# Performance work log

Measured on AMD Instinct MI355X. Metric: run time of the kernel, lower is better.

The kernel has to match this reference:

```python
import jax, jax.numpy as jnp
import numpy as np

S = 2048        # tokens (single prefill sequence)
HID = 3584      # hidden_size
H = 16          # num query heads
KV = 8          # num kv heads
D = 256         # head_dim
WINDOW = 1024   # sliding window size
CAP = 50.0      # logit softcap
SCALE = 256.0 ** -0.5   # query_pre_attn_scalar ** -0.5
THETA = 10000.0


def setup_inputs() -> dict:
    key = jax.random.key(0)
    ks = jax.random.split(key, 5)
    hidden_states = jax.random.normal(ks[0], (S, HID), dtype=jnp.float32)
    positions = jnp.arange(S, dtype=jnp.int32)
    Wq = jax.random.normal(ks[1], (HID, H * D), dtype=jnp.float32) * 0.02
    Wk = jax.random.normal(ks[2], (HID, KV * D), dtype=jnp.float32) * 0.02
    Wv = jax.random.normal(ks[3], (HID, KV * D), dtype=jnp.float32) * 0.02
    Wo = jax.random.normal(ks[4], (H * D, HID), dtype=jnp.float32) * 0.02
    return {"hidden_states": hidden_states, "positions": positions,
            "Wq": Wq, "Wk": Wk, "Wv": Wv, "Wo": Wo}


def _rope_neox(x, positions):
    # x: [S, n_heads, D]; neox-style: rotate halves, full rotary_dim == D
    half = D // 2
    inv_freq = 1.0 / (THETA ** (jnp.arange(0, half, dtype=jnp.float32) * 2.0 / D))
    freqs = positions.astype(jnp.float32)[:, None] * inv_freq[None, :]  # [S, half]
    cos = jnp.cos(freqs)[:, None, :].astype(x.dtype)
    sin = jnp.sin(freqs)[:, None, :].astype(x.dtype)
    x1, x2 = x[..., :half], x[..., half:]
    return jnp.concatenate([x1 * cos - x2 * sin, x2 * cos + x1 * sin], axis=-1)


def reference(hidden_states, positions, Wq, Wk, Wv, Wo):
    # QKV projections (no bias)
    q = (hidden_states @ Wq).reshape(S, H, D)
    k = (hidden_states @ Wk).reshape(S, KV, D)
    v = (hidden_states @ Wv).reshape(S, KV, D)
    q = _rope_neox(q, positions)
    k = _rope_neox(k, positions)
    # grouped-query attention: G query heads per kv head
    G = H // KV
    qg = q.reshape(S, KV, G, D)
    scores = jnp.einsum('qkgd,skd->kgqs', qg, k) * jnp.asarray(SCALE, q.dtype)
    # logit soft-capping
    scores = CAP * jnp.tanh(scores / CAP)
    # causal + sliding-window mask
    i = positions[:, None]
    j = positions[None, :]
    mask = (j <= i) & ((i - j) < WINDOW)   # [S, S]
    neg = jnp.finfo(scores.dtype).min
    scores = jnp.where(mask[None, None, :, :], scores, neg)
    p = jax.nn.softmax(scores, axis=-1)
    attn = jnp.einsum('kgqs,skd->qkgd', p, v).reshape(S, H * D)
    return attn @ Wo
```

## Files before the change

kernel.cpp:

```cpp
#include <hip/hip_runtime.h>
#include <stdint.h>

#define S 2048
#define HID 3584
#define NH 16
#define NKV 8
#define DH 256
#define WINDOW 1024
#define SCALE 0.0625f
#define CAP 50.0f

typedef short s16x8 __attribute__((ext_vector_type(8)));
typedef float f32x4 __attribute__((ext_vector_type(4)));

__device__ __forceinline__ short f2bf(float f) {
  union { float f; uint32_t u; } c; c.f = f;
  uint32_t u = c.u;
  uint32_t r = (u + 0x7FFFu + ((u >> 16) & 1u)) >> 16;
  return (short)r;
}
__device__ __forceinline__ float bf2f(short s) {
  union { uint32_t u; float f; } c;
  c.u = ((uint32_t)(uint16_t)s) << 16;
  return c.f;
}
__device__ __forceinline__ void gll16(const void* g, void* l) {
  __builtin_amdgcn_global_load_lds((const __attribute__((address_space(1))) void*)g,
                                   (__attribute__((address_space(3))) void*)l, 16, 0, 0);
}
#define BAR() asm volatile("s_barrier" ::: "memory")
#define VW6() asm volatile("s_waitcnt vmcnt(6)" ::: "memory")

__global__ void rope_table_kernel(float2* __restrict__ tbl) {
  int idx = blockIdx.x * 256 + threadIdx.x;
  int s = idx >> 7, i = idx & 127;
  float inv = __expf(-(float)i * (9.210340371976184f / 128.0f));
  float fr = (float)s * inv;
  tbl[idx] = make_float2(cosf(fr), sinf(fr));
}

__global__ void conv_hs_kernel(const float* __restrict__ src, short* __restrict__ dst) {
  int gid = blockIdx.x * 256 + threadIdx.x;
  float4 a = *(const float4*)&src[(size_t)gid * 8];
  float4 b = *(const float4*)&src[(size_t)gid * 8 + 4];
  s16x8 o;
  o[0] = f2bf(a.x); o[1] = f2bf(a.y); o[2] = f2bf(a.z); o[3] = f2bf(a.w);
  o[4] = f2bf(b.x); o[5] = f2bf(b.y); o[6] = f2bf(b.z); o[7] = f2bf(b.w);
  *(s16x8*)&dst[(size_t)gid * 8] = o;
}

__global__ __launch_bounds__(256)
void transpose_kernel(const float* __restrict__ src, short* __restrict__ dst,
                      int K, int N)
{
  __shared__ __align__(16) short t[64][76];
  int ntn = N >> 6;
  int tn = blockIdx.x % ntn, tk = blockIdx.x / ntn;
  int tid = threadIdx.x;
  int c = tid & 63, rg = tid >> 6;
  #pragma unroll
  for (int i = 0; i < 4; ++i) {
    int r0 = i * 16 + rg * 4;
    short tmp[4];
    #pragma unroll
    for (int j = 0; j < 4; ++j)
      tmp[j] = f2bf(src[(size_t)(tk * 64 + r0 + j) * N + tn * 64 + c]);
    *(short4*)&t[c][r0] = *(short4*)tmp;
  }
  __syncthreads();
  #pragma unroll
  for (int it = 0; it < 2; ++it) {
    int flat = it * 256 + tid;
    int n = flat >> 3, kc = flat & 7;
    *(s16x8*)&dst[(size_t)(tn * 64 + n) * K + tk * 64 + kc * 8] = *(s16x8*)&t[n][kc * 8];
  }
}

template<int BN, int KS>
__device__ __forceinline__ void gemm_ph(const short* __restrict__ srcA,
                                        const short* __restrict__ srcB,
                                        int tid, int NT,
                                        f32x4 (&acc)[8][BN / 64])
{
  constexpr int NFP = BN / 128;
  constexpr int BTILE = BN * 64;
  __shared__ __align__(16) short Asb[2 * 16384];
  __shared__ __align__(16) short Bsb[2 * BTILE];
  const int wv = tid >> 6, lane = tid & 63;
  const int lr = lane & 15, lk = lane >> 4;
  const int wm_id = wv >> 2, wn_id = wv & 3;
  const int r7 = lr & 7;
  const int abase = (wm_id * 128 + lr) * 64 + ((lk ^ r7) * 8);
  const int bbase = (wn_id * (BN / 4) + lr) * 64 + ((lk ^ r7) * 8);

  s16x8 af[4][2];
  s16x8 bfr[2][NFP][2];

  auto stA = [&](int ts, int r, int b) {
    gll16(srcA + (size_t)ts * 64 + (size_t)(r * 64) * KS,
          Asb + b * 16384 + r * 4096 + wv * 512);
  };
  auto stB = [&](int ts, int q, int b) {
    gll16(srcB + (size_t)ts * 64 + (size_t)(q * 64) * KS,
          Bsb + b * BTILE + q * 4096 + wv * 512);
  };
  auto LDA = [&](int mh, int b) {
    const short* A = Asb + b * 16384;
    #pragma unroll
    for (int mf = 0; mf < 4; ++mf)
      #pragma unroll
      for (int kh = 0; kh < 2; ++kh)
        af[mf][kh] = *(const s16x8*)&A[(abase + (mh * 64 + mf * 16) * 64) ^ (kh * 32)];
  };
  auto LDB = [&](int nh, int b) {
    const short* B = Bsb + b * BTILE;
    #pragma unroll
    for (int nf = 0; nf < NFP; ++nf)
      #pragma unroll
      for (int kh = 0; kh < 2; ++kh)
        bfr[nh][nf][kh] = *(const s16x8*)&B[(bbase + (nh * NFP + nf) * 16 * 64) ^ (kh * 32)];
  };
  auto MMA = [&](int mh, int nh) {
    asm volatile("s_waitcnt lgkmcnt(0)" ::: "memory");
    __builtin_amdgcn_sched_barrier(0);
    __builtin_amdgcn_s_setprio(1);
    #pragma unroll
    for (int mf = 0; mf < 4; ++mf)
      #pragma unroll
      for (int nf = 0; nf < NFP; ++nf) {
        acc[mh * 4 + mf][nh * NFP + nf] =
          __builtin_amdgcn_mfma_f32_16x16x32_bf16(af[mf][0], bfr[nh][nf][0],
                                                  acc[mh * 4 + mf][nh * NFP + nf], 0, 0, 0);
        acc[mh * 4 + mf][nh * NFP + nf] =
          __builtin_amdgcn_mfma_f32_16x16x32_bf16(af[mf][1], bfr[nh][nf][1],
                                                  acc[mh * 4 + mf][nh * NFP + nf], 0, 0, 0);
      }
    __builtin_amdgcn_s_setprio(0);
  };

  #pragma unroll
  for (int r = 0; r < 4; ++r) stA(0, r, 0);
  #pragma unroll
  for (int q = 0; q < BN / 64; ++q) stB(0, q, 0);
  #pragma unroll
  for (int r = 0; r < 4; ++r) stA(1, r, 1);
  stB(1, 0, 1); stB(1, 1, 1);
  asm volatile("s_waitcnt vmcnt(0)" ::: "memory");
  BAR();

  const int NI = NT / 2;
  for (int i = 0; i < NI; ++i) {
    const int T = 2 * i;
    const int t2 = (T + 2 < NT) ? T + 2 : NT - 2;
    const int t3 = (T + 3 < NT) ? T + 3 : NT - 1;
    LDA(0, 0); LDB(0, 0);
    if constexpr (BN == 256) { stB(T + 1, 2, 1); stB(T + 1, 3, 1); }
    BAR(); MMA(0, 0); BAR();
    LDB(1, 0);
    stA(t2, 0, 0); stA(t2, 2, 0);
    BAR(); MMA(0, 1); BAR();
    LDA(1, 0);
    stB(t2, 0, 0); stB(t2, 1, 0);
    BAR(); MMA(1, 0); BAR();
    stA(t2, 1, 0); stA(t2, 3, 0);
    VW6();
    BAR(); MMA(1, 1); BAR();
    LDA(0, 1); LDB(0, 1);
    if constexpr (BN == 256) { stB(t2, 2, 0); stB(t2, 3, 0); }
    BAR(); MMA(0, 0); BAR();
    LDB(1, 1);
    stA(t3, 0, 1); stA(t3, 2, 1);
    BAR(); MMA(0, 1); BAR();
    LDA(1, 1);
    stB(t3, 0, 1); stB(t3, 1, 1);
    BAR(); MMA(1, 0); BAR();
    stA(t3, 1, 1); stA(t3, 3, 1);
    VW6();
    BAR(); MMA(1, 1); BAR();
  }
  asm volatile("s_waitcnt vmcnt(0)" ::: "memory");
}

__global__ __launch_bounds__(512, 2)
void qkv_gemm8_kernel(const short* __restrict__ hsb, const short* __restrict__ Wt,
                      short* __restrict__ qb, short* __restrict__ kbuf,
                      short* __restrict__ vtb)
{
  int bid = blockIdx.x;
  int swz = (bid & 7) * 32 + (bid >> 3);
  int bm = swz >> 5, bn = swz & 31;
  int m0 = bm * 256, n0 = bn * 256;
  int tid = threadIdx.x;
  int row8 = tid >> 3;
  int colsw = ((tid & 7) ^ (row8 & 7)) * 8;
  const short* srcA = hsb + (size_t)(m0 + row8) * HID + colsw;
  const short* srcB = Wt + (size_t)(n0 + row8) * HID + colsw;
  f32x4 acc[8][4] = {};
  gemm_ph<256, HID>(srcA, srcB, tid, HID / 64, acc);

  int wv = tid >> 6, lane = tid & 63;
  int lr = lane & 15, lk = lane >> 4;
  int wm = (wv >> 2) * 128, wn = (wv & 3) * 64;
  int region = (n0 < 4096) ? 0 : ((n0 < 6144) ? 1 : 2);
  #pragma unroll
  for (int m = 0; m < 8; ++m) {
    int srow_b = m0 + wm + m * 16 + lk * 4;
    #pragma unroll
    for (int n = 0; n < 4; ++n) {
      int ncol = n0 + wn + n * 16 + lr;
      #pragma unroll
      for (int r = 0; r < 4; ++r) {
        int srow = srow_b + r;
        short bv = f2bf(acc[m][n][r]);
        if (region == 0) {
          int h = ncol >> 8, d = ncol & 255;
          qb[((size_t)h * S + srow) * DH + d] = bv;
        } else if (region == 1) {
          int c = ncol - 4096; int kv = c >> 8, d = c & 255;
          kbuf[((size_t)kv * S + srow) * DH + d] = bv;
        } else {
          int c = ncol - 6144; int kv = c >> 8, d = c & 255;
          vtb[((size_t)kv * DH + d) * S + srow] = bv;
        }
      }
    }
  }
}

__global__ __launch_bounds__(512, 2)
void out_gemm8_kernel(const short* __restrict__ attnb, const short* __restrict__ WtO,
                      float* __restrict__ out)
{
  int bid = blockIdx.x;
  int swz = (bid & 7) * 28 + (bid >> 3);
  int bm = swz / 28, bn = swz % 28;
  int m0 = bm * 256, n0 = bn * 128;
  int tid = threadIdx.x;
  int row8 = tid >> 3;
  int colsw = ((tid & 7) ^ (row8 & 7)) * 8;
  const short* srcA = attnb + (size_t)(m0 + row8) * 4096 + colsw;
  const short* srcB = WtO + (size_t)(n0 + row8) * 4096 + colsw;
  f32x4 acc[8][2] = {};
  gemm_ph<128, 4096>(srcA, srcB, tid, 4096 / 64, acc);

  int wv = tid >> 6, lane = tid & 63;
  int lr = lane & 15, lk = lane >> 4;
  int wm = (wv >> 2) * 128, wn = (wv & 3) * 32;
  #pragma unroll
  for (int m = 0; m < 8; ++m) {
    int srow_b = m0 + wm + m * 16 + lk * 4;
    #pragma unroll
    for (int n = 0; n < 2; ++n) {
      int ncol = n0 + wn + n * 16 + lr;
      #pragma unroll
      for (int r = 0; r < 4; ++r)
        out[(size_t)(srow_b + r) * HID + ncol] = acc[m][n][r];
    }
  }
}

__global__ void rope_kernel(short* __restrict__ qb, short* __restrict__ kbuf,
                            const float2* __restrict__ tbl)
{
  int gid = blockIdx.x * 256 + threadIdx.x;
  int row = gid >> 4, ch = gid & 15;
  short* base = (row < NH * S) ? (qb + (size_t)row * DH)
                               : (kbuf + (size_t)(row - NH * S) * DH);
  int s = row & (S - 1);
  int i0 = ch * 8;
  s16x8 x1 = *(s16x8*)(base + i0);
  s16x8 x2 = *(s16x8*)(base + 128 + i0);
  s16x8 y1, y2;
  #pragma unroll
  for (int j = 0; j < 8; ++j) {
    float2 cs = tbl[s * 128 + i0 + j];
    float a = bf2f(x1[j]), b = bf2f(x2[j]);
    y1[j] = f2bf(a * cs.x - b * cs.y);
    y2[j] = f2bf(b * cs.x + a * cs.y);
  }
  *(s16x8*)(base + i0) = y1;
  *(s16x8*)(base + 128 + i0) = y2;
}

__global__ __launch_bounds__(256)
void attn_kernel(const short* __restrict__ qb, const short* __restrict__ kbuf,
                 const short* __restrict__ vtb, short* __restrict__ attnb)
{
  __shared__ __align__(16) short Klds[64][256];
  __shared__ __align__(16) short Vlds[256][72];
  __shared__ __align__(16) short Plds[4][16][76];
  int bid = blockIdx.x;
  int qt = bid >> 4, h = bid & 15;
  int kv = h >> 1;
  int q0 = qt * 64;
  int tid = threadIdx.x, w = tid >> 6, lane = tid & 63;
  int lr = lane & 15, lk = lane >> 4;
  int qrow_base = q0 + w * 16;
  s16x8 qf[8];
  const short* qrow = qb + ((size_t)h * S + (qrow_base + lr)) * DH;
  #pragma unroll
  for (int kb = 0; kb < 8; ++kb)
    qf[kb] = *(const s16x8*)(qrow + kb * 32 + lk * 8);
  f32x4 acc_o[16] = {};
  float l_r[4] = {0.0f, 0.0f, 0.0f, 0.0f};
  int tlo = (q0 >= WINDOW - 1) ? ((q0 - (WINDOW - 1)) >> 6) : 0;
  int thi = q0 >> 6;
  const short* kbase = kbuf + (size_t)kv * S * DH;
  const short* vbase = vtb + (size_t)kv * DH * S;

  s16x8 kpf[8], vpf[8];
  auto loadRegs = [&](int t) {
    int k0 = t * 64;
    #pragma unroll
    for (int it = 0; it < 8; ++it) {
      int flat = it * 256 + tid;
      int r = flat >> 5, cg = flat & 31;
      kpf[it] = *(const s16x8*)(kbase + (size_t)(k0 + r) * DH + cg * 8);
    }
    #pragma unroll
    for (int it = 0; it < 8; ++it) {
      int flat = it * 256 + tid;
      int r = flat >> 3, cg = flat & 7;
      vpf[it] = *(const s16x8*)(vbase + (size_t)r * S + k0 + cg * 8);
    }
  };
  auto writeLds = [&]() {
    #pragma unroll
    for (int it = 0; it < 8; ++it) {
      int flat = it * 256 + tid;
      int r = flat >> 5, cg = flat & 31;
      *(s16x8*)&Klds[r][(cg ^ (r & 7)) * 8] = kpf[it];
    }
    #pragma unroll
    for (int it = 0; it < 8; ++it) {
      int flat = it * 256 + tid;
      int r = flat >> 3, cg = flat & 7;
      *(s16x8*)&Vlds[r][cg * 8] = vpf[it];
    }
  };

  loadRegs(tlo);
  for (int t = tlo; t <= thi; ++t) {
    int k0 = t * 64;
    writeLds();
    __syncthreads();
    if (t < thi) loadRegs(t + 1);
    f32x4 sc4[4] = {};
    __builtin_amdgcn_s_setprio(1);
    #pragma unroll
    for (int kb = 0; kb < 8; ++kb)
      #pragma unroll
      for (int ni = 0; ni < 4; ++ni) {
        int row = ni * 16 + lr;
        s16x8 b = *(const s16x8*)&Klds[row][(((kb << 2) | lk) ^ (row & 7)) * 8];
        sc4[ni] = __builtin_amdgcn_mfma_f32_16x16x32_bf16(qf[kb], b, sc4[ni], 0, 0, 0);
      }
    __builtin_amdgcn_s_setprio(0);
    bool interior = (k0 + 63 <= qrow_base) && (qrow_base + 15 - k0 < WINDOW);
    #pragma unroll
    for (int ni = 0; ni < 4; ++ni)
      #pragma unroll
      for (int r = 0; r < 4; ++r) {
        float raw = sc4[ni][r];
        float u = fabsf(raw) * (2.0f * SCALE / CAP);
        float e = __expf(-u);
        float th = (1.0f - e) / (1.0f + e);
        float z = CAP * copysignf(th, raw) - CAP;
        if (!interior) {
          int qg = qrow_base + lk * 4 + r;
          int kg = k0 + ni * 16 + lr;
          bool valid = (kg <= qg) && (qg - kg < WINDOW);
          z = valid ? z : -1e30f;
        }
        float p = __expf(z);
        sc4[ni][r] = p;
        l_r[r] += p;
      }
    #pragma unroll
    for (int ni = 0; ni < 4; ++ni)
      #pragma unroll
      for (int r = 0; r < 4; ++r)
        Plds[w][lk * 4 + r][ni * 16 + lr] = f2bf(sc4[ni][r]);
    s16x8 pa0 = *(const s16x8*)&Plds[w][lr][lk * 8];
    s16x8 pa1 = *(const s16x8*)&Plds[w][lr][32 + lk * 8];
    __builtin_amdgcn_s_setprio(1);
    #pragma unroll
    for (int df = 0; df < 16; ++df) {
      s16x8 b0 = *(const s16x8*)&Vlds[df * 16 + lr][lk * 8];
      s16x8 b1 = *(const s16x8*)&Vlds[df * 16 + lr][32 + lk * 8];
      acc_o[df] = __builtin_amdgcn_mfma_f32_16x16x32_bf16(pa0, b0, acc_o[df], 0, 0, 0);
      acc_o[df] = __builtin_amdgcn_mfma_f32_16x16x32_bf16(pa1, b1, acc_o[df], 0, 0, 0);
    }
    __builtin_amdgcn_s_setprio(0);
    __syncthreads();
  }
  #pragma unroll
  for (int r = 0; r < 4; ++r) {
    float lsum = l_r[r];
    #pragma unroll
    for (int off = 1; off < 16; off <<= 1)
      lsum += __shfl_xor(lsum, off, 64);
    float inv = 1.0f / lsum;
    int srow = qrow_base + lk * 4 + r;
    #pragma unroll
    for (int df = 0; df < 16; ++df)
      attnb[(size_t)srow * (NH * DH) + h * DH + df * 16 + lr] = f2bf(acc_o[df][r] * inv);
  }
}

extern "C" void kernel_launch(void* const* d_in, const int* in_sizes, int n_in,
                              void* d_out, int out_size, void* d_ws, size_t ws_size,
                              hipStream_t stream) {
  const float* hs = (const float*)d_in[0];
  const float* Wq = (const float*)d_in[2];
  const float* Wk = (const float*)d_in[3];
  const float* Wv = (const float*)d_in[4];
  const float* Wo = (const float*)d_in[5];
  float* out = (float*)d_out;
  char* ws = (char*)d_ws;
  size_t off = 0;
  float2* tbl  = (float2*)(ws + off); off += 2097152;
  short* qb    = (short*)(ws + off);  off += 16777216;
  short* kbuf  = (short*)(ws + off);  off += 8388608;
  short* vtb   = (short*)(ws + off);  off += 8388608;
  short* attnb = (short*)(ws + off);  off += 16777216;
  short* hsb   = (short*)(ws + off);  off += 14680064;
  short* Wt    = (short*)(ws + off);  off += 58720256;
  short* WtO   = (short*)(ws + off);  off += 29360128;

  hipLaunchKernelGGL(rope_table_kernel, dim3(1024), dim3(256), 0, stream, tbl);
  hipLaunchKernelGGL(conv_hs_kernel, dim3(3584), dim3(256), 0, stream, hs, hsb);
  hipLaunchKernelGGL(transpose_kernel, dim3(64 * 56), dim3(256), 0, stream,
                     Wq, Wt, HID, 4096);
  hipLaunchKernelGGL(transpose_kernel, dim3(32 * 56), dim3(256), 0, stream,
                     Wk, Wt + (size_t)4096 * HID, HID, 2048);
  hipLaunchKernelGGL(transpose_kernel, dim3(32 * 56), dim3(256), 0, stream,
                     Wv, Wt + (size_t)6144 * HID, HID, 2048);
  hipLaunchKernelGGL(transpose_kernel, dim3(56 * 64), dim3(256), 0, stream,
                     Wo, WtO, 4096, HID);
  hipLaunchKernelGGL(qkv_gemm8_kernel, dim3(256), dim3(512), 0, stream,
                     hsb, Wt, qb, kbuf, vtb);
  hipLaunchKernelGGL(rope_kernel, dim3(3072), dim3(256), 0, stream, qb, kbuf, tbl);
  hipLaunchKernelGGL(attn_kernel, dim3(512), dim3(256), 0, stream,
                     qb, kbuf, vtb, attnb);
  hipLaunchKernelGGL(out_gemm8_kernel, dim3(224), dim3(512), 0, stream,
                     attnb, WtO, out);
}
```

Baseline: 408.6 us.

## Double-buffer LDS fragment registers to overlap LDS reads with MFMA

The GEMM main loop now keeps two sets of A and B fragment registers. It issues the LDS reads for the next MMA sub-block before running the current MFMA batch, and drops the explicit lgkmcnt(0) wait at the start of each MMA. The aim is to hide LDS read latency behind matrix-core work instead of stalling before each batch. In exchange, more live fragment registers raise VGPR pressure under the 512x2 launch bound, which could cause spills or lower occupancy. Correctness now relies on compiler-inserted waits and on the buffer-reuse ordering across barriers.

```diff
diff --git a/kernel.cpp b/kernel.cpp
--- a/kernel.cpp
+++ b/kernel.cpp
@@ -93,8 +93,8 @@
   const int abase = (wm_id * 128 + lr) * 64 + ((lk ^ r7) * 8);
   const int bbase = (wn_id * (BN / 4) + lr) * 64 + ((lk ^ r7) * 8);
 
-  s16x8 af[4][2];
-  s16x8 bfr[2][NFP][2];
+  s16x8 afA[4][2], afB[4][2];
+  s16x8 bf0[NFP][2], bf1[NFP][2];
 
   auto stA = [&](int ts, int r, int b) {
     gll16(srcA + (size_t)ts * 64 + (size_t)(r * 64) * KS,
@@ -104,24 +104,23 @@
     gll16(srcB + (size_t)ts * 64 + (size_t)(q * 64) * KS,
           Bsb + b * BTILE + q * 4096 + wv * 512);
   };
-  auto LDA = [&](int mh, int b) {
+  auto RDA = [&](s16x8 (&dst)[4][2], int mh, int b) {
     const short* A = Asb + b * 16384;
     #pragma unroll
     for (int mf = 0; mf < 4; ++mf)
       #pragma unroll
       for (int kh = 0; kh < 2; ++kh)
-        af[mf][kh] = *(const s16x8*)&A[(abase + (mh * 64 + mf * 16) * 64) ^ (kh * 32)];
-  };
-  auto LDB = [&](int nh, int b) {
+        dst[mf][kh] = *(const s16x8*)&A[(abase + (mh * 64 + mf * 16) * 64) ^ (kh * 32)];
+  };
+  auto RDB = [&](s16x8 (&dst)[NFP][2], int nh, int b) {
     const short* B = Bsb + b * BTILE;
     #pragma unroll
     for (int nf = 0; nf < NFP; ++nf)
       #pragma unroll
       for (int kh = 0; kh < 2; ++kh)
-        bfr[nh][nf][kh] = *(const s16x8*)&B[(bbase + (nh * NFP + nf) * 16 * 64) ^ (kh * 32)];
-  };
-  auto MMA = [&](int mh, int nh) {
-    asm volatile("s_waitcnt lgkmcnt(0)" ::: "memory");
+        dst[nf][kh] = *(const s16x8*)&B[(bbase + (nh * NFP + nf) * 16 * 64) ^ (kh * 32)];
+  };
+  auto MMA = [&](s16x8 (&fa)[4][2], s16x8 (&fb)[NFP][2], int mh, int nh) {
     __builtin_amdgcn_sched_barrier(0);
     __builtin_amdgcn_s_setprio(1);
     #pragma unroll
@@ -129,10 +128,10 @@
       #pragma unroll
       for (int nf = 0; nf < NFP; ++nf) {
         acc[mh * 4 + mf][nh * NFP + nf] =
-          __builtin_amdgcn_mfma_f32_16x16x32_bf16(af[mf][0], bfr[nh][nf][0],
+          __builtin_amdgcn_mfma_f32_16x16x32_bf16(fa[mf][0], fb[nf][0],
                                                   acc[mh * 4 + mf][nh * NFP + nf], 0, 0, 0);
         acc[mh * 4 + mf][nh * NFP + nf] =
-          __builtin_amdgcn_mfma_f32_16x16x32_bf16(af[mf][1], bfr[nh][nf][1],
+          __builtin_amdgcn_mfma_f32_16x16x32_bf16(fa[mf][1], fb[nf][1],
                                                   acc[mh * 4 + mf][nh * NFP + nf], 0, 0, 0);
       }
     __builtin_amdgcn_s_setprio(0);
@@ -147,36 +146,53 @@
   stB(1, 0, 1); stB(1, 1, 1);
   asm volatile("s_waitcnt vmcnt(0)" ::: "memory");
   BAR();
+  RDA(afA, 0, 0); RDB(bf0, 0, 0);
 
   const int NI = NT / 2;
   for (int i = 0; i < NI; ++i) {
     const int T = 2 * i;
     const int t2 = (T + 2 < NT) ? T + 2 : NT - 2;
     const int t3 = (T + 3 < NT) ? T + 3 : NT - 1;
-    LDA(0, 0); LDB(0, 0);
     if constexpr (BN == 256) { stB(T + 1, 2, 1); stB(T + 1, 3, 1); }
-    BAR(); MMA(0, 0); BAR();
-    LDB(1, 0);
+    BAR();
+    RDB(bf1, 1, 0);
+    MMA(afA, bf0, 0, 0);
+    BAR();
     stA(t2, 0, 0); stA(t2, 2, 0);
-    BAR(); MMA(0, 1); BAR();
-    LDA(1, 0);
+    BAR();
+    RDA(afB, 1, 0);
+    MMA(afA, bf1, 0, 1);
+    BAR();
     stB(t2, 0, 0); stB(t2, 1, 0);
-    BAR(); MMA(1, 0); BAR();
+    BAR();
+    MMA(afB, bf0, 1, 0);
+    BAR();
     stA(t2, 1, 0); stA(t2, 3, 0);
     VW6();
-    BAR(); MMA(1, 1); BAR();
-    LDA(0, 1); LDB(0, 1);
+    BAR();
+    RDA(afA, 0, 1); RDB(bf0, 0, 1);
+    MMA(afB, bf1, 1, 1);
+    BAR();
     if constexpr (BN == 256) { stB(t2, 2, 0); stB(t2, 3, 0); }
-    BAR(); MMA(0, 0); BAR();
-    LDB(1, 1);
+    BAR();
+    RDB(bf1, 1, 1);
+    MMA(afA, bf0, 0, 0);
+    BAR();
     stA(t3, 0, 1); stA(t3, 2, 1);
-    BAR(); MMA(0, 1); BAR();
-    LDA(1, 1);
+    BAR();
+    RDA(afB, 1, 1);
+    MMA(afA, bf1, 0, 1);
+    BAR();
     stB(t3, 0, 1); stB(t3, 1, 1);
-    BAR(); MMA(1, 0); BAR();
+    BAR();
+    MMA(afB, bf0, 1, 0);
+    BAR();
     stA(t3, 1, 1); stA(t3, 3, 1);
     VW6();
-    BAR(); MMA(1, 1); BAR();
+    BAR();
+    RDA(afA, 0, 0); RDB(bf0, 0, 0);
+    MMA(afB, bf1, 1, 1);
+    BAR();
   }
   asm volatile("s_waitcnt vmcnt(0)" ::: "memory");
 }
```

After: 418.4 us. 2.4% more time.

## Split attention key tiles across two wave groups per block and merge results

Applied to the files above, without the earlier changes.

Each attention block now runs 512 threads split into two groups of four waves. The groups process alternating key tiles of the same query tile in separate LDS buffers, then combine their partial outputs and row sums through LDS at the end. This halves the serial key-tile loop per block to cut per-block latency. It also reverses the query-tile order so the heaviest tiles launch first, and swizzles the V LDS layout. The costs are double the LDS footprint, an extra combine pass, and possible register pressure or occupancy limits under the 512-thread launch bound.

```diff
diff --git a/kernel.cpp b/kernel.cpp
--- a/kernel.cpp
+++ b/kernel.cpp
@@ -282,20 +282,23 @@
   *(s16x8*)(base + 128 + i0) = y2;
 }
 
-__global__ __launch_bounds__(256)
+__global__ __launch_bounds__(512)
 void attn_kernel(const short* __restrict__ qb, const short* __restrict__ kbuf,
                  const short* __restrict__ vtb, short* __restrict__ attnb)
 {
-  __shared__ __align__(16) short Klds[64][256];
-  __shared__ __align__(16) short Vlds[256][72];
-  __shared__ __align__(16) short Plds[4][16][76];
+  __shared__ __align__(16) short Klds[2][64][256];
+  __shared__ __align__(16) short Vlds[2][256][72];
+  __shared__ __align__(16) short Plds[8][16][72];
   int bid = blockIdx.x;
-  int qt = bid >> 4, h = bid & 15;
+  int qt = 31 - (bid >> 4), h = bid & 15;
   int kv = h >> 1;
   int q0 = qt * 64;
-  int tid = threadIdx.x, w = tid >> 6, lane = tid & 63;
+  int tid = threadIdx.x;
+  int w = tid >> 6, lane = tid & 63;
+  int g = w >> 2, wsub = w & 3;
+  int gtid = tid & 255;
   int lr = lane & 15, lk = lane >> 4;
-  int qrow_base = q0 + w * 16;
+  int qrow_base = q0 + wsub * 16;
   s16x8 qf[8];
   const short* qrow = qb + ((size_t)h * S + (qrow_base + lr)) * DH;
   #pragma unroll
@@ -313,13 +316,13 @@
     int k0 = t * 64;
     #pragma unroll
     for (int it = 0; it < 8; ++it) {
-      int flat = it * 256 + tid;
+      int flat = it * 256 + gtid;
       int r = flat >> 5, cg = flat & 31;
       kpf[it] = *(const s16x8*)(kbase + (size_t)(k0 + r) * DH + cg * 8);
     }
     #pragma unroll
     for (int it = 0; it < 8; ++it) {
-      int flat = it * 256 + tid;
+      int flat = it * 256 + gtid;
       int r = flat >> 3, cg = flat & 7;
       vpf[it] = *(const s16x8*)(vbase + (size_t)r * S + k0 + cg * 8);
     }
@@ -327,84 +330,117 @@
   auto writeLds = [&]() {
     #pragma unroll
     for (int it = 0; it < 8; ++it) {
-      int flat = it * 256 + tid;
+      int flat = it * 256 + gtid;
       int r = flat >> 5, cg = flat & 31;
-      *(s16x8*)&Klds[r][(cg ^ (r & 7)) * 8] = kpf[it];
+      *(s16x8*)&Klds[g][r][(cg ^ (r & 7)) * 8] = kpf[it];
     }
     #pragma unroll
     for (int it = 0; it < 8; ++it) {
-      int flat = it * 256 + tid;
+      int flat = it * 256 + gtid;
       int r = flat >> 3, cg = flat & 7;
-      *(s16x8*)&Vlds[r][cg * 8] = vpf[it];
-    }
-  };
-
-  loadRegs(tlo);
-  for (int t = tlo; t <= thi; ++t) {
-    int k0 = t * 64;
-    writeLds();
+      *(s16x8*)&Vlds[g][r][(cg ^ (r & 7)) * 8] = vpf[it];
+    }
+  };
+
+  int tg0 = tlo + g;
+  int n_all = thi - tlo + 1;
+  int jmax = (n_all + 1) >> 1;
+  if (tg0 <= thi) loadRegs(tg0);
+  for (int j = 0; j < jmax; ++j) {
+    int t = tg0 + 2 * j;
+    bool active = (t <= thi);
+    if (active) writeLds();
     __syncthreads();
-    if (t < thi) loadRegs(t + 1);
-    f32x4 sc4[4] = {};
-    __builtin_amdgcn_s_setprio(1);
-    #pragma unroll
-    for (int kb = 0; kb < 8; ++kb)
-      #pragma unroll
-      for (int ni = 0; ni < 4; ++ni) {
-        int row = ni * 16 + lr;
-        s16x8 b = *(const s16x8*)&Klds[row][(((kb << 2) | lk) ^ (row & 7)) * 8];
-        sc4[ni] = __builtin_amdgcn_mfma_f32_16x16x32_bf16(qf[kb], b, sc4[ni], 0, 0, 0);
+    if (active && t + 2 <= thi) loadRegs(t + 2);
+    if (active) {
+      int k0 = t * 64;
+      f32x4 sc4[4] = {};
+      __builtin_amdgcn_s_setprio(1);
+      #pragma unroll
+      for (int kb = 0; kb < 8; ++kb)
+        #pragma unroll
+        for (int ni = 0; ni < 4; ++ni) {
+          int row = ni * 16 + lr;
+          s16x8 b = *(const s16x8*)&Klds[g][row][(((kb << 2) | lk) ^ (row & 7)) * 8];
+          sc4[ni] = __builtin_amdgcn_mfma_f32_16x16x32_bf16(qf[kb], b, sc4[ni], 0, 0, 0);
+        }
+      __builtin_amdgcn_s_setprio(0);
+      bool interior = (k0 + 63 <= qrow_base) && (qrow_base + 15 - k0 < WINDOW);
+      #pragma unroll
+      for (int ni = 0; ni < 4; ++ni)
+        #pragma unroll
+        for (int r = 0; r < 4; ++r) {
+          float raw = sc4[ni][r];
+          float u = fabsf(raw) * (2.0f * SCALE / CAP);
+          float e = __expf(-u);
+          float th = (1.0f - e) / (1.0f + e);
+          float z = CAP * copysignf(th, raw) - CAP;
+          if (!interior) {
+            int qg = qrow_base + lk * 4 + r;
+            int kg = k0 + ni * 16 + lr;
+            bool valid = (kg <= qg) && (qg - kg < WINDOW);
+            z = valid ? z : -1e30f;
+          }
+          float p = __expf(z);
+          sc4[ni][r] = p;
+          l_r[r] += p;
+        }
+      #pragma unroll
+      for (int ni = 0; ni < 4; ++ni)
+        #pragma unroll
+        for (int r = 0; r < 4; ++r)
+          Plds[w][lk * 4 + r][ni * 16 + lr] = f2bf(sc4[ni][r]);
+      s16x8 pa0 = *(const s16x8*)&Plds[w][lr][lk * 8];
+      s16x8 pa1 = *(const s16x8*)&Plds[w][lr][32 + lk * 8];
+      __builtin_amdgcn_s_setprio(1);
+      #pragma unroll
+      for (int df = 0; df < 16; ++df) {
+        int row = df * 16 + lr;
+        s16x8 b0 = *(const s16x8*)&Vlds[g][row][((lk ^ (row & 7)) * 8)];
+        s16x8 b1 = *(const s16x8*)&Vlds[g][row][(((4 + lk) ^ (row & 7)) * 8)];
+        acc_o[df] = __builtin_amdgcn_mfma_f32_16x16x32_bf16(pa0, b0, acc_o[df], 0, 0, 0);
+        acc_o[df] = __builtin_amdgcn_mfma_f32_16x16x32_bf16(pa1, b1, acc_o[df], 0, 0, 0);
       }
-    __builtin_amdgcn_s_setprio(0);
-    bool interior = (k0 + 63 <= qrow_base) && (qrow_base + 15 - k0 < WINDOW);
-    #pragma unroll
-    for (int ni = 0; ni < 4; ++ni)
-      #pragma unroll
-      for (int r = 0; r < 4; ++r) {
-        float raw = sc4[ni][r];
-        float u = fabsf(raw) * (2.0f * SCALE / CAP);
-        float e = __expf(-u);
-        float th = (1.0f - e) / (1.0f + e);
-        float z = CAP * copysignf(th, raw) - CAP;
-        if (!interior) {
-          int qg = qrow_base + lk * 4 + r;
-          int kg = k0 + ni * 16 + lr;
-          bool valid = (kg <= qg) && (qg - kg < WINDOW);
-          z = valid ? z : -1e30f;
-        }
-        float p = __expf(z);
-        sc4[ni][r] = p;
-        l_r[r] += p;
+      __builtin_amdgcn_s_setprio(0);
+    }
+    __syncthreads();
+  }
+  float lsum[4];
+  #pragma unroll
+  for (int r = 0; r < 4; ++r) {
+    float v = l_r[r];
+    #pragma unroll
+    for (int off = 1; off < 16; off <<= 1)
+      v += __shfl_xor(v, off, 64);
+    lsum[r] = v;
+  }
+  float* comb = (float*)&Klds[0][0][0];
+  float* lcomb = (float*)&Vlds[0][0][0];
+  if (g == 1) {
+    #pragma unroll
+    for (int df = 0; df < 16; ++df)
+      #pragma unroll
+      for (int r = 0; r < 4; ++r)
+        comb[(size_t)(wsub * 16 + lk * 4 + r) * 256 + df * 16 + lr] = acc_o[df][r];
+    if (lr == 0)
+      #pragma unroll
+      for (int r = 0; r < 4; ++r)
+        lcomb[wsub * 16 + lk * 4 + r] = lsum[r];
+  }
+  __syncthreads();
+  if (g == 0) {
+    #pragma unroll
+    for (int r = 0; r < 4; ++r) {
+      int rowi = wsub * 16 + lk * 4 + r;
+      float lt = lsum[r] + lcomb[rowi];
+      float inv = 1.0f / lt;
+      int srow = q0 + rowi;
+      #pragma unroll
+      for (int df = 0; df < 16; ++df) {
+        float o = acc_o[df][r] + comb[(size_t)rowi * 256 + df * 16 + lr];
+        attnb[(size_t)srow * (NH * DH) + h * DH + df * 16 + lr] = f2bf(o * inv);
       }
-    #pragma unroll
-    for (int ni = 0; ni < 4; ++ni)
-      #pragma unroll
-      for (int r = 0; r < 4; ++r)
-        Plds[w][lk * 4 + r][ni * 16 + lr] = f2bf(sc4[ni][r]);
-    s16x8 pa0 = *(const s16x8*)&Plds[w][lr][lk * 8];
-    s16x8 pa1 = *(const s16x8*)&Plds[w][lr][32 + lk * 8];
-    __builtin_amdgcn_s_setprio(1);
-    #pragma unroll
-    for (int df = 0; df < 16; ++df) {
-      s16x8 b0 = *(const s16x8*)&Vlds[df * 16 + lr][lk * 8];
-      s16x8 b1 = *(const s16x8*)&Vlds[df * 16 + lr][32 + lk * 8];
-      acc_o[df] = __builtin_amdgcn_mfma_f32_16x16x32_bf16(pa0, b0, acc_o[df], 0, 0, 0);
-      acc_o[df] = __builtin_amdgcn_mfma_f32_16x16x32_bf16(pa1, b1, acc_o[df], 0, 0, 0);
-    }
-    __builtin_amdgcn_s_setprio(0);
-    __syncthreads();
-  }
-  #pragma unroll
-  for (int r = 0; r < 4; ++r) {
-    float lsum = l_r[r];
-    #pragma unroll
-    for (int off = 1; off < 16; off <<= 1)
-      lsum += __shfl_xor(lsum, off, 64);
-    float inv = 1.0f / lsum;
-    int srow = qrow_base + lk * 4 + r;
-    #pragma unroll
-    for (int df = 0; df < 16; ++df)
-      attnb[(size_t)srow * (NH * DH) + h * DH + df * 16 + lr] = f2bf(acc_o[df][r] * inv);
+    }
   }
 }
 
@@ -441,7 +477,7 @@
   hipLaunchKernelGGL(qkv_gemm8_kernel, dim3(256), dim3(512), 0, stream,
                      hsb, Wt, qb, kbuf, vtb);
   hipLaunchKernelGGL(rope_kernel, dim3(3072), dim3(256), 0, stream, qb, kbuf, tbl);
-  hipLaunchKernelGGL(attn_kernel, dim3(512), dim3(256), 0, stream,
+  hipLaunchKernelGGL(attn_kernel, dim3(512), dim3(512), 0, stream,
                      qb, kbuf, vtb, attnb);
   hipLaunchKernelGGL(out_gemm8_kernel, dim3(224), dim3(512), 0, stream,
                      attnb, WtO, out);
```

After: 405.3 us. No clear change (-0.8%).
